# Optimization experiments

Measured on AMD Instinct MI355X. Metric: run time of the kernel, lower is better.

Reference implementation:

```python
import jax, jax.numpy as jnp
import numpy as np

B, T, C = 4, 2048, 2048
N_HEAD = 16
HEAD_DIM = C // N_HEAD
ROPE_BASE = 10000.0


def setup_inputs() -> dict:
    key = jax.random.key(0)
    k1, k2, k3 = jax.random.split(key, 3)
    x = jax.random.normal(k1, (B, T, C), dtype=jnp.float32)
    w_attn = jax.random.normal(k2, (3 * C, C), dtype=jnp.float32) * (1.0 / np.sqrt(C))
    w_proj = jax.random.normal(k3, (C, C), dtype=jnp.float32) * (1.0 / np.sqrt(C))
    return {"x": x, "w_attn": w_attn, "w_proj": w_proj}


def _apply_rope(x, cos, sin):
    # x: [B, H, T, hd]; interleaved pairs (even, odd) rotated
    x_ = x.reshape(*x.shape[:-1], -1, 2)
    x0, x1 = x_[..., 0], x_[..., 1]
    x0r = x0 * cos - x1 * sin
    x1r = x0 * sin + x1 * cos
    return jnp.stack([x0r, x1r], axis=-1).reshape(x.shape)


def reference(x, w_attn, w_proj):
    Bx, Tx, Cx = x.shape
    hd = Cx // N_HEAD
    d = hd // 2

    qkv = jnp.einsum('btc,fc->btf', x, w_attn)  # [B,T,3C]
    q, k, v = jnp.split(qkv, 3, axis=-1)

    def to_heads(t):
        return t.reshape(Bx, Tx, N_HEAD, hd).transpose(0, 2, 1, 3)  # [B,H,T,hd]

    q, k, v = to_heads(q), to_heads(k), to_heads(v)

    # RoPE
    theta = 1.0 / (ROPE_BASE ** (2.0 * jnp.arange(d, dtype=jnp.float32) / hd))
    t = jnp.arange(Tx, dtype=x.dtype)
    freqs = jnp.outer(t, theta.astype(x.dtype))  # [T, d]
    cos = jnp.cos(freqs)[None, None]  # [1,1,T,d]
    sin = jnp.sin(freqs)[None, None]
    q = _apply_rope(q, cos, sin)
    k = _apply_rope(k, cos, sin)

    # Causal attention
    scale = 1.0 / jnp.sqrt(jnp.asarray(hd, dtype=x.dtype))
    scores = jnp.einsum('bhqd,bhkd->bhqk', q, k) * scale
    causal = jnp.tril(jnp.ones((Tx, Tx), dtype=bool))
    scores = jnp.where(causal[None, None], scores, jnp.asarray(-jnp.inf, dtype=scores.dtype))
    attn = jax.nn.softmax(scores, axis=-1)
    y = jnp.einsum('bhqk,bhkd->bhqd', attn, v)  # [B,H,T,hd]

    y = y.transpose(0, 2, 1, 3).reshape(Bx, Tx, Cx)
    return jnp.einsum('btc,oc->bto', y, w_proj)
```

## Files before the change

kernel.cpp:

```cpp
#include <hip/hip_runtime.h>

#define B_ 4
#define T_ 2048
#define C_ 2048
#define H_ 16
#define N1_ 6144
#define M_ 8192
#define SCALE_ 0.08838834764831845f

typedef unsigned short u16;
typedef __bf16 bf16x8 __attribute__((ext_vector_type(8)));
typedef float f32x4 __attribute__((ext_vector_type(4)));
typedef float f32x16 __attribute__((ext_vector_type(16)));

__device__ __forceinline__ u16 f2bf(float f) {
  union { float f; unsigned u; } v; v.f = f;
  return (u16)((v.u + 0x7fffu + ((v.u >> 16) & 1u)) >> 16);
}
__device__ __forceinline__ float bf2f(u16 h) {
  union { unsigned u; float f; } v; v.u = ((unsigned)h) << 16;
  return v.f;
}

__device__ __forceinline__ void gld16(const void* g, void* l) {
  __builtin_amdgcn_global_load_lds(
      (__attribute__((address_space(1))) unsigned int*)(unsigned long long)g,
      (__attribute__((address_space(3))) unsigned int*)(unsigned)(unsigned long long)l,
      16, 0, 0);
}

__global__ void k_cast(const float* __restrict__ in, u16* __restrict__ out, int n4) {
  int i = blockIdx.x * 256 + threadIdx.x;
  if (i >= n4) return;
  float4 v = reinterpret_cast<const float4*>(in)[i];
  ushort4 o;
  o.x = f2bf(v.x); o.y = f2bf(v.y); o.z = f2bf(v.z); o.w = f2bf(v.w);
  reinterpret_cast<ushort4*>(out)[i] = o;
}

__global__ void k_trig(float2* __restrict__ trig) {
  int idx = blockIdx.x * 256 + threadIdx.x;
  int t = idx >> 6, i = idx & 63;
  float theta = __expf(-(float)i * 0.14391156831212787f);
  float f = (float)t * theta;
  float s, c;
  sincosf(f, &s, &c);
  trig[idx] = make_float2(c, s);
}

__global__ void k_rope(u16* __restrict__ qh, u16* __restrict__ kh,
                       const float2* __restrict__ trig) {
  int idx = blockIdx.x * 256 + threadIdx.x;
  u16* base = (idx >> 21) ? kh : qh;
  int c = idx & ((1 << 21) - 1);
  int t = (c >> 4) & (T_ - 1);
  int i0 = (c & 15) << 2;
  u16* p = base + ((size_t)c << 3);
  ushort4 a = *reinterpret_cast<ushort4*>(p);
  ushort4 bq = *reinterpret_cast<ushort4*>(p + 4);
  const float2* tr = trig + t * 64 + i0;
  float2 t0 = tr[0], t1 = tr[1], t2 = tr[2], t3 = tr[3];
  float x0, x1;
  ushort4 ra, rb;
  x0 = bf2f(a.x); x1 = bf2f(a.y);
  ra.x = f2bf(x0 * t0.x - x1 * t0.y); ra.y = f2bf(x0 * t0.y + x1 * t0.x);
  x0 = bf2f(a.z); x1 = bf2f(a.w);
  ra.z = f2bf(x0 * t1.x - x1 * t1.y); ra.w = f2bf(x0 * t1.y + x1 * t1.x);
  x0 = bf2f(bq.x); x1 = bf2f(bq.y);
  rb.x = f2bf(x0 * t2.x - x1 * t2.y); rb.y = f2bf(x0 * t2.y + x1 * t2.x);
  x0 = bf2f(bq.z); x1 = bf2f(bq.w);
  rb.z = f2bf(x0 * t3.x - x1 * t3.y); rb.w = f2bf(x0 * t3.y + x1 * t3.x);
  *reinterpret_cast<ushort4*>(p) = ra;
  *reinterpret_cast<ushort4*>(p + 4) = rb;
}

template <int EPI>
__global__ __launch_bounds__(256, 2) void k_gemm(
    const u16* __restrict__ A, const u16* __restrict__ Bt,
    float* __restrict__ Cf,
    u16* __restrict__ qh, u16* __restrict__ kh, u16* __restrict__ vt,
    int Ndim, int K) {
  __shared__ alignas(16) u16 lA[128 * 32];
  __shared__ alignas(16) u16 lB[128 * 32];
  const int tid = threadIdx.x;
  const int lane = tid & 63;
  const int w = tid >> 6;
  const int wr = w >> 1, wc = w & 1;
  const int l15 = lane & 15, lq = lane >> 4;
  const long rowBase = (long)blockIdx.y * 128;
  const long colBase = (long)blockIdx.x * 128;

  const f32x4 z4 = {0.f, 0.f, 0.f, 0.f};
  f32x4 acc[4][4];
#pragma unroll
  for (int m = 0; m < 4; ++m)
#pragma unroll
    for (int n = 0; n < 4; ++n) acc[m][n] = z4;

  for (int k0 = 0; k0 < K; k0 += 32) {
#pragma unroll
    for (int i = 0; i < 2; ++i) {
      int c = tid + i * 256;
      int r = c >> 2, e = (c & 3) << 3;
      gld16(A + (rowBase + r) * (long)K + k0 + e, (char*)lA + c * 16);
      gld16(Bt + (colBase + r) * (long)K + k0 + e, (char*)lB + c * 16);
    }
    __syncthreads();
    bf16x8 aF[4], bF[4];
#pragma unroll
    for (int m = 0; m < 4; ++m)
      aF[m] = *reinterpret_cast<const bf16x8*>(&lA[(wr * 64 + m * 16 + l15) * 32 + lq * 8]);
#pragma unroll
    for (int n = 0; n < 4; ++n)
      bF[n] = *reinterpret_cast<const bf16x8*>(&lB[(wc * 64 + n * 16 + l15) * 32 + lq * 8]);
#pragma unroll
    for (int m = 0; m < 4; ++m)
#pragma unroll
      for (int n = 0; n < 4; ++n)
        acc[m][n] = __builtin_amdgcn_mfma_f32_16x16x32_bf16(aF[m], bF[n], acc[m][n], 0, 0, 0);
    __syncthreads();
  }

  if (EPI == 0) {
#pragma unroll
    for (int m = 0; m < 4; ++m) {
      long row0 = rowBase + wr * 64 + m * 16 + lq * 4;
#pragma unroll
      for (int n = 0; n < 4; ++n) {
        long col = colBase + wc * 64 + n * 16 + l15;
#pragma unroll
        for (int j = 0; j < 4; ++j)
          Cf[(row0 + j) * (long)Ndim + col] = acc[m][n][j];
      }
    }
  } else {
    const int sec = (int)(colBase >> 11);
    const int hh = ((int)colBase >> 7) & 15;
#pragma unroll
    for (int m = 0; m < 4; ++m) {
      int row0 = (int)rowBase + wr * 64 + m * 16 + lq * 4;
      int b = row0 >> 11;
      int t0 = row0 & (T_ - 1);
      long bh = (long)b * H_ + hh;
#pragma unroll
      for (int n = 0; n < 4; ++n) {
        int dd = wc * 64 + n * 16 + l15;
        if (sec < 2) {
          u16* dst = sec ? kh : qh;
#pragma unroll
          for (int j = 0; j < 4; ++j)
            dst[(bh * T_ + t0 + j) * 128 + dd] = f2bf(acc[m][n][j]);
        } else {
          ushort4 pk;
          pk.x = f2bf(acc[m][n][0]); pk.y = f2bf(acc[m][n][1]);
          pk.z = f2bf(acc[m][n][2]); pk.w = f2bf(acc[m][n][3]);
          *reinterpret_cast<ushort4*>(&vt[(bh * 128 + dd) * T_ + t0]) = pk;
        }
      }
    }
  }
}

#define PACK_SLOT(dst, P, base)                                                       \
  {                                                                                   \
    unsigned ua, ub, uc, ud;                                                          \
    asm("v_cvt_pk_bf16_f32 %0, %1, %2" : "=v"(ua) : "v"(P[base + 0]), "v"(P[base + 1])); \
    asm("v_cvt_pk_bf16_f32 %0, %1, %2" : "=v"(ub) : "v"(P[base + 4]), "v"(P[base + 5])); \
    asm("v_permlane32_swap_b32 %0, %1" : "+v"(ua), "+v"(ub));                         \
    asm("v_cvt_pk_bf16_f32 %0, %1, %2" : "=v"(uc) : "v"(P[base + 2]), "v"(P[base + 3])); \
    asm("v_cvt_pk_bf16_f32 %0, %1, %2" : "=v"(ud) : "v"(P[base + 6]), "v"(P[base + 7])); \
    asm("v_permlane32_swap_b32 %0, %1" : "+v"(uc), "+v"(ud));                         \
    union { unsigned u[4]; bf16x8 v; } tt;                                            \
    tt.u[0] = ua; tt.u[1] = uc; tt.u[2] = ub; tt.u[3] = ud;                           \
    dst = tt.v;                                                                       \
  }

__global__ __launch_bounds__(256, 2) void k_attn(
    const u16* __restrict__ qh, const u16* __restrict__ kh,
    const u16* __restrict__ vt, u16* __restrict__ ym) {
  __shared__ alignas(16) u16 lK[2][64 * 128];
  __shared__ alignas(16) u16 lV[2][128 * 64];
  const int tid = threadIdx.x;
  const int lane = tid & 63;
  const int w = tid >> 6;
  const int l31 = lane & 31;
  const int hi = lane >> 5;
  const int swz = (l31 & 7) << 4;
  const int id = (int)blockIdx.x;
  const int pr = id >> 6;
  const int bh = ((id & 7) << 3) | ((id >> 3) & 7);
  const int b = bh >> 4, hh = bh & 15;
  const u16* Kbase = kh + (long)bh * T_ * 128;
  const u16* Vbase = vt + (long)bh * 128 * T_;
  const u16* Qbase = qh + (long)bh * T_ * 128;

  auto stage = [&](int bi, int t0) {
#pragma unroll
    for (int i = 0; i < 4; ++i) {
      int c = tid + i * 256;
      int rK = c >> 4;
      int lbK = ((c & 15) << 4) ^ ((rK & 7) << 4);
      gld16(Kbase + (long)(t0 + rK) * 128 + (lbK >> 1), (char*)(&lK[bi][0]) + c * 16);
      int dV = c >> 3;
      int lbV = ((c & 7) << 4) ^ ((dV & 7) << 4);
      gld16(Vbase + (long)dV * T_ + t0 + (lbV >> 1), (char*)(&lV[bi][0]) + c * 16);
    }
  };

#pragma unroll 1
  for (int half = 0; half < 2; ++half) {
    const int p = half ? 15 - pr : pr;
    const int NT = 2 * (p + 1);
    const int qw = p * 128 + w * 32;
    const int ntw = (qw + 95) >> 6;

    bf16x8 qF[8];
    {
      const u16* qrow = Qbase + (long)(qw + l31) * 128 + hi * 8;
#pragma unroll
      for (int s = 0; s < 8; ++s)
        qF[s] = *reinterpret_cast<const bf16x8*>(qrow + s * 16);
    }

    f32x16 oA[4];
#pragma unroll
    for (int n = 0; n < 4; ++n)
#pragma unroll
      for (int r = 0; r < 16; ++r) oA[n][r] = 0.f;
    float mR = -1e30f, lR = 0.f;

    stage(0, 0);
    __syncthreads();
    int cur = 0;
#pragma unroll 1
    for (int jt = 0; jt < NT; ++jt) {
      if (jt + 1 < NT) stage(cur ^ 1, (jt + 1) * 64);
      if (jt < ntw) {
        const int t0 = jt * 64;
        const char* Kc = (const char*)(&lK[cur][0]);
        const char* Vc = (const char*)(&lV[cur][0]);
        f32x16 s0, s1;
#pragma unroll
        for (int r = 0; r < 16; ++r) { s0[r] = 0.f; s1[r] = 0.f; }
        __builtin_amdgcn_s_setprio(1);
#pragma unroll
        for (int s = 0; s < 8; ++s) {
          int cb = (s * 32 + hi * 16) ^ swz;
          bf16x8 k0 = *reinterpret_cast<const bf16x8*>(Kc + l31 * 256 + cb);
          bf16x8 k1 = *reinterpret_cast<const bf16x8*>(Kc + (32 + l31) * 256 + cb);
          s0 = __builtin_amdgcn_mfma_f32_32x32x16_bf16(k0, qF[s], s0, 0, 0, 0);
          s1 = __builtin_amdgcn_mfma_f32_32x32x16_bf16(k1, qF[s], s1, 0, 0, 0);
        }
        __builtin_amdgcn_s_setprio(0);

        float f0[16], f1[16];
#pragma unroll
        for (int r = 0; r < 16; ++r) { f0[r] = s0[r] * SCALE_; f1[r] = s1[r] * SCALE_; }
        if (jt == ntw - 1) {
          const int qa = qw + l31;
#pragma unroll
          for (int r = 0; r < 16; ++r) {
            int kv = t0 + (r & 3) + 8 * (r >> 2) + 4 * hi;
            if (kv > qa) f0[r] = -1e30f;
            if (kv + 32 > qa) f1[r] = -1e30f;
          }
        }
        float mt = fmaxf(f0[0], f1[0]);
#pragma unroll
        for (int r = 1; r < 16; ++r) mt = fmaxf(mt, fmaxf(f0[r], f1[r]));
        mt = fmaxf(mt, __shfl_xor(mt, 32));
        float mN = fmaxf(mR, mt);
        float al = __expf(mR - mN);
        mR = mN;
        float rs = 0.f;
#pragma unroll
        for (int r = 0; r < 16; ++r) {
          f0[r] = __expf(f0[r] - mN);
          f1[r] = __expf(f1[r] - mN);
          rs += f0[r] + f1[r];
        }
        rs += __shfl_xor(rs, 32);
        lR = lR * al + rs;
        float aR[16];
#pragma unroll
        for (int r = 0; r < 16; ++r)
          aR[r] = __shfl(al, (r & 3) + 8 * (r >> 2) + 4 * hi);
#pragma unroll
        for (int n = 0; n < 4; ++n)
#pragma unroll
          for (int r = 0; r < 16; ++r) oA[n][r] *= aR[r];

        bf16x8 paF[4];
        PACK_SLOT(paF[0], f0, 0);
        PACK_SLOT(paF[1], f0, 8);
        PACK_SLOT(paF[2], f1, 0);
        PACK_SLOT(paF[3], f1, 8);

        __builtin_amdgcn_s_setprio(1);
#pragma unroll
        for (int n = 0; n < 4; ++n) {
          const char* vrow = Vc + (n * 32 + l31) * 128;
#pragma unroll
          for (int ks = 0; ks < 4; ++ks) {
            bf16x8 bV = *reinterpret_cast<const bf16x8*>(vrow + ((ks * 32 + hi * 16) ^ swz));
            oA[n] = __builtin_amdgcn_mfma_f32_32x32x16_bf16(paF[ks], bV, oA[n], 0, 0, 0);
          }
        }
        __builtin_amdgcn_s_setprio(0);
      }
      __syncthreads();
      cur ^= 1;
    }

    float li = 1.f / lR;
    float liR[16];
#pragma unroll
    for (int r = 0; r < 16; ++r)
      liR[r] = __shfl(li, (r & 3) + 8 * (r >> 2) + 4 * hi);
    u16* yrow = ym + ((long)b * T_ + qw) * C_ + hh * 128 + l31;
#pragma unroll
    for (int n = 0; n < 4; ++n)
#pragma unroll
      for (int r = 0; r < 16; ++r) {
        int cr = (r & 3) + 8 * (r >> 2) + 4 * hi;
        yrow[(long)cr * C_ + n * 32] = f2bf(oA[n][r] * liR[r]);
      }
  }
}

extern "C" void kernel_launch(void* const* d_in, const int* in_sizes, int n_in,
                              void* d_out, int out_size, void* d_ws, size_t ws_size,
                              hipStream_t stream) {
  (void)in_sizes; (void)n_in; (void)out_size; (void)ws_size;
  const float* x = (const float*)d_in[0];
  const float* wa = (const float*)d_in[1];
  const float* wp = (const float*)d_in[2];
  float* out = (float*)d_out;
  char* ws = (char*)d_ws;

  size_t off = 0;
  auto alloc = [&](size_t bytes) -> char* {
    char* p = ws + off;
    off += (bytes + 255) & ~(size_t)255;
    return p;
  };
  u16* xb  = (u16*)alloc((size_t)M_ * C_ * 2);
  u16* wab = (u16*)alloc((size_t)N1_ * C_ * 2);
  u16* wpb = (u16*)alloc((size_t)C_ * C_ * 2);
  u16* qh  = (u16*)alloc((size_t)64 * T_ * 128 * 2);
  u16* kh  = (u16*)alloc((size_t)64 * T_ * 128 * 2);
  u16* vt  = (u16*)alloc((size_t)64 * 128 * T_ * 2);
  float2* trig = (float2*)alloc((size_t)T_ * 64 * 8);
  u16* ym = xb;

  k_cast<<<dim3((M_ * C_ / 4) / 256), 256, 0, stream>>>(x, xb, M_ * C_ / 4);
  k_cast<<<dim3((N1_ * C_ / 4) / 256), 256, 0, stream>>>(wa, wab, N1_ * C_ / 4);
  k_cast<<<dim3((C_ * C_ / 4) / 256), 256, 0, stream>>>(wp, wpb, C_ * C_ / 4);
  k_trig<<<dim3((T_ * 64) / 256), 256, 0, stream>>>(trig);
  k_gemm<1><<<dim3(N1_ / 128, M_ / 128), 256, 0, stream>>>(
      xb, wab, nullptr, qh, kh, vt, N1_, C_);
  k_rope<<<dim3((2 * 64 * T_ * 16) / 256), 256, 0, stream>>>(qh, kh, trig);
  k_attn<<<dim3(512), 256, 0, stream>>>(qh, kh, vt, ym);
  k_gemm<0><<<dim3(C_ / 128, M_ / 128), 256, 0, stream>>>(
      ym, wpb, out, nullptr, nullptr, nullptr, C_, C_);
}
```

Baseline: 493.6 us.

## Rewrite GEMM as 256x128 triple-buffered pipelined kernel and fuse RoPE into epilogue

Replaces the 128x128, single-buffered, 32-wide-K GEMM with an 8-wave 256x128 tile. It uses a 3-stage LDS ring over 64-wide K slices, issues async global-to-LDS loads interleaved with MFMA phases, and controls ordering with explicit vmcnt waits, barriers and s_setprio. LDS rows are XOR-swizzled to avoid bank conflicts, and blocks are remapped with a grouped swizzle to improve L2 reuse. RoPE is folded into the QKV GEMM epilogue using a lane-pair shuffle, which removes the separate read-modify-write rope kernel. The kernel now hardcodes K=2048 and uses about 144KB of LDS per block, which limits occupancy to one block per CU.

```diff
diff --git a/kernel.cpp b/kernel.cpp
--- a/kernel.cpp
+++ b/kernel.cpp
@@ -48,47 +48,28 @@
   trig[idx] = make_float2(c, s);
 }
 
-__global__ void k_rope(u16* __restrict__ qh, u16* __restrict__ kh,
-                       const float2* __restrict__ trig) {
-  int idx = blockIdx.x * 256 + threadIdx.x;
-  u16* base = (idx >> 21) ? kh : qh;
-  int c = idx & ((1 << 21) - 1);
-  int t = (c >> 4) & (T_ - 1);
-  int i0 = (c & 15) << 2;
-  u16* p = base + ((size_t)c << 3);
-  ushort4 a = *reinterpret_cast<ushort4*>(p);
-  ushort4 bq = *reinterpret_cast<ushort4*>(p + 4);
-  const float2* tr = trig + t * 64 + i0;
-  float2 t0 = tr[0], t1 = tr[1], t2 = tr[2], t3 = tr[3];
-  float x0, x1;
-  ushort4 ra, rb;
-  x0 = bf2f(a.x); x1 = bf2f(a.y);
-  ra.x = f2bf(x0 * t0.x - x1 * t0.y); ra.y = f2bf(x0 * t0.y + x1 * t0.x);
-  x0 = bf2f(a.z); x1 = bf2f(a.w);
-  ra.z = f2bf(x0 * t1.x - x1 * t1.y); ra.w = f2bf(x0 * t1.y + x1 * t1.x);
-  x0 = bf2f(bq.x); x1 = bf2f(bq.y);
-  rb.x = f2bf(x0 * t2.x - x1 * t2.y); rb.y = f2bf(x0 * t2.y + x1 * t2.x);
-  x0 = bf2f(bq.z); x1 = bf2f(bq.w);
-  rb.z = f2bf(x0 * t3.x - x1 * t3.y); rb.w = f2bf(x0 * t3.y + x1 * t3.x);
-  *reinterpret_cast<ushort4*>(p) = ra;
-  *reinterpret_cast<ushort4*>(p + 4) = rb;
-}
-
 template <int EPI>
-__global__ __launch_bounds__(256, 2) void k_gemm(
+__global__ __launch_bounds__(512, 2) void k_gemm8(
     const u16* __restrict__ A, const u16* __restrict__ Bt,
     float* __restrict__ Cf,
     u16* __restrict__ qh, u16* __restrict__ kh, u16* __restrict__ vt,
-    int Ndim, int K) {
-  __shared__ alignas(16) u16 lA[128 * 32];
-  __shared__ alignas(16) u16 lB[128 * 32];
+    const float2* __restrict__ trig, int nbx, int cpx) {
+  __shared__ alignas(16) u16 lA[3 * 256 * 64];
+  __shared__ alignas(16) u16 lB[3 * 128 * 64];
   const int tid = threadIdx.x;
   const int lane = tid & 63;
   const int w = tid >> 6;
   const int wr = w >> 1, wc = w & 1;
   const int l15 = lane & 15, lq = lane >> 4;
-  const long rowBase = (long)blockIdx.y * 128;
-  const long colBase = (long)blockIdx.x * 128;
+  const int rs = l15 & 7;
+
+  const int id = (int)blockIdx.x;
+  const int swz = (id & 7) * cpx + (id >> 3);
+  const int bx = swz % nbx, by = swz / nbx;
+  const long rowBase = (long)by * 256;
+  const long colBase = (long)bx * 128;
+  const u16* Ag = A + rowBase * 2048;
+  const u16* Bg = Bt + colBase * 2048;
 
   const f32x4 z4 = {0.f, 0.f, 0.f, 0.f};
   f32x4 acc[4][4];
@@ -97,28 +78,99 @@
 #pragma unroll
     for (int n = 0; n < 4; ++n) acc[m][n] = z4;
 
-  for (int k0 = 0; k0 < K; k0 += 32) {
-#pragma unroll
-    for (int i = 0; i < 2; ++i) {
-      int c = tid + i * 256;
-      int r = c >> 2, e = (c & 3) << 3;
-      gld16(A + (rowBase + r) * (long)K + k0 + e, (char*)lA + c * 16);
-      gld16(Bt + (colBase + r) * (long)K + k0 + e, (char*)lB + c * 16);
-    }
-    __syncthreads();
+#pragma unroll
+  for (int pt = 0; pt < 2; ++pt) {
+    char* Ad = (char*)lA + pt * 32768;
+    char* Bd = (char*)lB + pt * 16384;
+    const long kG = (long)pt * 64;
+#pragma unroll
+    for (int q = 0; q < 4; ++q) {
+      int c = tid + q * 512;
+      gld16(Ag + (long)(c >> 3) * 2048 + kG + (((c & 7) ^ ((c >> 3) & 7)) << 3),
+            Ad + c * 16);
+    }
+#pragma unroll
+    for (int q = 0; q < 2; ++q) {
+      int c = tid + q * 512;
+      gld16(Bg + (long)(c >> 3) * 2048 + kG + (((c & 7) ^ ((c >> 3) & 7)) << 3),
+            Bd + c * 16);
+    }
+  }
+  asm volatile("s_waitcnt vmcnt(6)" ::: "memory");
+  __builtin_amdgcn_s_barrier();
+
+  int slot = 0;
+#pragma unroll 1
+  for (int t = 0; t < 32; ++t) {
+    const char* As = (const char*)lA + slot * 32768;
+    const char* Bs = (const char*)lB + slot * 16384;
+    int s2 = slot + 2; if (s2 >= 3) s2 -= 3;
+    char* Ad = (char*)lA + s2 * 32768;
+    char* Bd = (char*)lB + s2 * 16384;
+    const long kG = (long)(t + 2) * 64;
+    const bool st = (t < 30);
+
     bf16x8 aF[4], bF[4];
 #pragma unroll
-    for (int m = 0; m < 4; ++m)
-      aF[m] = *reinterpret_cast<const bf16x8*>(&lA[(wr * 64 + m * 16 + l15) * 32 + lq * 8]);
-#pragma unroll
-    for (int n = 0; n < 4; ++n)
-      bF[n] = *reinterpret_cast<const bf16x8*>(&lB[(wc * 64 + n * 16 + l15) * 32 + lq * 8]);
-#pragma unroll
-    for (int m = 0; m < 4; ++m)
-#pragma unroll
-      for (int n = 0; n < 4; ++n)
-        acc[m][n] = __builtin_amdgcn_mfma_f32_16x16x32_bf16(aF[m], bF[n], acc[m][n], 0, 0, 0);
-    __syncthreads();
+    for (int fm = 0; fm < 4; ++fm)
+      aF[fm] = *reinterpret_cast<const bf16x8*>(
+          As + (wr * 64 + fm * 16 + l15) * 128 + ((lq ^ rs) << 4));
+#pragma unroll
+    for (int fn = 0; fn < 4; ++fn)
+      bF[fn] = *reinterpret_cast<const bf16x8*>(
+          Bs + (wc * 64 + fn * 16 + l15) * 128 + ((lq ^ rs) << 4));
+    if (st) {
+#pragma unroll
+      for (int q = 0; q < 3; ++q) {
+        int c = tid + q * 512;
+        gld16(Ag + (long)(c >> 3) * 2048 + kG + (((c & 7) ^ ((c >> 3) & 7)) << 3),
+              Ad + c * 16);
+      }
+    }
+    __builtin_amdgcn_s_barrier();
+    __builtin_amdgcn_s_setprio(1);
+#pragma unroll
+    for (int fm = 0; fm < 4; ++fm)
+#pragma unroll
+      for (int fn = 0; fn < 4; ++fn)
+        acc[fm][fn] =
+            __builtin_amdgcn_mfma_f32_16x16x32_bf16(aF[fm], bF[fn], acc[fm][fn], 0, 0, 0);
+    __builtin_amdgcn_s_setprio(0);
+    __builtin_amdgcn_s_barrier();
+#pragma unroll
+    for (int fm = 0; fm < 4; ++fm)
+      aF[fm] = *reinterpret_cast<const bf16x8*>(
+          As + (wr * 64 + fm * 16 + l15) * 128 + (((4 | lq) ^ rs) << 4));
+#pragma unroll
+    for (int fn = 0; fn < 4; ++fn)
+      bF[fn] = *reinterpret_cast<const bf16x8*>(
+          Bs + (wc * 64 + fn * 16 + l15) * 128 + (((4 | lq) ^ rs) << 4));
+    if (st) {
+      {
+        int c = tid + 1536;
+        gld16(Ag + (long)(c >> 3) * 2048 + kG + (((c & 7) ^ ((c >> 3) & 7)) << 3),
+              Ad + c * 16);
+      }
+#pragma unroll
+      for (int q = 0; q < 2; ++q) {
+        int c = tid + q * 512;
+        gld16(Bg + (long)(c >> 3) * 2048 + kG + (((c & 7) ^ ((c >> 3) & 7)) << 3),
+              Bd + c * 16);
+      }
+    }
+    __builtin_amdgcn_s_barrier();
+    __builtin_amdgcn_s_setprio(1);
+#pragma unroll
+    for (int fm = 0; fm < 4; ++fm)
+#pragma unroll
+      for (int fn = 0; fn < 4; ++fn)
+        acc[fm][fn] =
+            __builtin_amdgcn_mfma_f32_16x16x32_bf16(aF[fm], bF[fn], acc[fm][fn], 0, 0, 0);
+    __builtin_amdgcn_s_setprio(0);
+    if (st) asm volatile("s_waitcnt vmcnt(6)" ::: "memory");
+    else    asm volatile("s_waitcnt vmcnt(0)" ::: "memory");
+    __builtin_amdgcn_s_barrier();
+    slot = (slot == 2) ? 0 : slot + 1;
   }
 
   if (EPI == 0) {
@@ -130,7 +182,7 @@
         long col = colBase + wc * 64 + n * 16 + l15;
 #pragma unroll
         for (int j = 0; j < 4; ++j)
-          Cf[(row0 + j) * (long)Ndim + col] = acc[m][n][j];
+          Cf[(row0 + j) * 2048 + col] = acc[m][n][j];
       }
     }
   } else {
@@ -148,8 +200,13 @@
         if (sec < 2) {
           u16* dst = sec ? kh : qh;
 #pragma unroll
-          for (int j = 0; j < 4; ++j)
-            dst[(bh * T_ + t0 + j) * 128 + dd] = f2bf(acc[m][n][j]);
+          for (int j = 0; j < 4; ++j) {
+            float v = acc[m][n][j];
+            float vp = __shfl_xor(v, 1);
+            float2 cs = trig[(t0 + j) * 64 + (dd >> 1)];
+            float r = (dd & 1) ? (vp * cs.y + v * cs.x) : (v * cs.x - vp * cs.y);
+            dst[(bh * T_ + t0 + j) * 128 + dd] = f2bf(r);
+          }
         } else {
           ushort4 pk;
           pk.x = f2bf(acc[m][n][0]); pk.y = f2bf(acc[m][n][1]);
@@ -357,10 +414,9 @@
   k_cast<<<dim3((N1_ * C_ / 4) / 256), 256, 0, stream>>>(wa, wab, N1_ * C_ / 4);
   k_cast<<<dim3((C_ * C_ / 4) / 256), 256, 0, stream>>>(wp, wpb, C_ * C_ / 4);
   k_trig<<<dim3((T_ * 64) / 256), 256, 0, stream>>>(trig);
-  k_gemm<1><<<dim3(N1_ / 128, M_ / 128), 256, 0, stream>>>(
-      xb, wab, nullptr, qh, kh, vt, N1_, C_);
-  k_rope<<<dim3((2 * 64 * T_ * 16) / 256), 256, 0, stream>>>(qh, kh, trig);
+  k_gemm8<1><<<dim3(1536), 512, 0, stream>>>(
+      xb, wab, nullptr, qh, kh, vt, trig, 48, 192);
   k_attn<<<dim3(512), 256, 0, stream>>>(qh, kh, vt, ym);
-  k_gemm<0><<<dim3(C_ / 128, M_ / 128), 256, 0, stream>>>(
-      ym, wpb, out, nullptr, nullptr, nullptr, C_, C_);
-}
+  k_gemm8<0><<<dim3(512), 512, 0, stream>>>(
+      ym, wpb, out, nullptr, nullptr, nullptr, nullptr, 16, 64);
+}
```

After: 463.3 us. -6.1%, faster.

## Replace GEMMs with 256x256 double-buffered pipelined kernel and fuse RoPE epilogue

Applied to the files above, without the earlier changes.

Replaces the simple 128x128 single-stage GEMM with a 512-thread 256x256 tile kernel using 64-wide K tiles, XOR-swizzled LDS, double-buffered async global-to-LDS staging interleaved with MFMA phases, s_setprio, and a grouped block-index swizzle for L2 reuse. RoPE is folded into the QKV GEMM epilogue using lane shuffles to fetch the pair partner, removing the separate rope kernel and its extra read/write pass over q and k. This trades much higher register and LDS pressure (128 KB LDS per block) and hardcoded K=2048 for better data reuse and latency hiding.

```diff
diff --git a/kernel.cpp b/kernel.cpp
--- a/kernel.cpp
+++ b/kernel.cpp
@@ -48,112 +48,144 @@
   trig[idx] = make_float2(c, s);
 }
 
-__global__ void k_rope(u16* __restrict__ qh, u16* __restrict__ kh,
-                       const float2* __restrict__ trig) {
-  int idx = blockIdx.x * 256 + threadIdx.x;
-  u16* base = (idx >> 21) ? kh : qh;
-  int c = idx & ((1 << 21) - 1);
-  int t = (c >> 4) & (T_ - 1);
-  int i0 = (c & 15) << 2;
-  u16* p = base + ((size_t)c << 3);
-  ushort4 a = *reinterpret_cast<ushort4*>(p);
-  ushort4 bq = *reinterpret_cast<ushort4*>(p + 4);
-  const float2* tr = trig + t * 64 + i0;
-  float2 t0 = tr[0], t1 = tr[1], t2 = tr[2], t3 = tr[3];
-  float x0, x1;
-  ushort4 ra, rb;
-  x0 = bf2f(a.x); x1 = bf2f(a.y);
-  ra.x = f2bf(x0 * t0.x - x1 * t0.y); ra.y = f2bf(x0 * t0.y + x1 * t0.x);
-  x0 = bf2f(a.z); x1 = bf2f(a.w);
-  ra.z = f2bf(x0 * t1.x - x1 * t1.y); ra.w = f2bf(x0 * t1.y + x1 * t1.x);
-  x0 = bf2f(bq.x); x1 = bf2f(bq.y);
-  rb.x = f2bf(x0 * t2.x - x1 * t2.y); rb.y = f2bf(x0 * t2.y + x1 * t2.x);
-  x0 = bf2f(bq.z); x1 = bf2f(bq.w);
-  rb.z = f2bf(x0 * t3.x - x1 * t3.y); rb.w = f2bf(x0 * t3.y + x1 * t3.x);
-  *reinterpret_cast<ushort4*>(p) = ra;
-  *reinterpret_cast<ushort4*>(p + 4) = rb;
-}
+
+#define STAGE_H(BUF, AB, HALF, KT, GSH)                                          \
+  {                                                                              \
+    _Pragma("unroll") for (int q = 0; q < 2; ++q) {                              \
+      int c = tid + q * 512;                                                     \
+      int idx = c >> 3;                                                          \
+      int row = (idx & ((1 << (GSH)) - 1)) + ((HALF) << (GSH)) +                 \
+                ((idx >> (GSH)) << ((GSH) + 1));                                 \
+      gld16(((AB) ? Bg : Ag) + (long)row * 2048 + (long)(KT) * 64 +              \
+                (((c & 7) ^ (idx & 7)) << 3),                                    \
+            (char*)&lds[BUF][AB][row * 64 + (c & 7) * 8]);                       \
+    }                                                                            \
+  }
+
+#define PHASE(BUF, MH, NH, RDA, RDB, STAGE_CODE, WAIT_CODE)                      \
+  {                                                                              \
+    if (RDA) {                                                                   \
+      _Pragma("unroll") for (int fr = 0; fr < 4; ++fr)                           \
+        _Pragma("unroll") for (int ks = 0; ks < 2; ++ks)                         \
+          aCur[fr][ks] = *reinterpret_cast<const bf16x8*>(                       \
+              &lds[BUF][0][(wm * 128 + (MH) * 64 + fr * 16 + l15) * 64 +         \
+                           (((ks * 4 + lq) ^ swl) << 3)]);                       \
+    }                                                                            \
+    if (RDB) {                                                                   \
+      _Pragma("unroll") for (int fc = 0; fc < 2; ++fc)                           \
+        _Pragma("unroll") for (int ks = 0; ks < 2; ++ks)                         \
+          bKp[NH][fc][ks] = *reinterpret_cast<const bf16x8*>(                    \
+              &lds[BUF][1][(wn * 64 + (NH) * 32 + fc * 16 + l15) * 64 +          \
+                           (((ks * 4 + lq) ^ swl) << 3)]);                       \
+    }                                                                            \
+    STAGE_CODE;                                                                  \
+    __builtin_amdgcn_s_barrier();                                                \
+    __builtin_amdgcn_s_setprio(1);                                               \
+    _Pragma("unroll") for (int fr = 0; fr < 4; ++fr)                             \
+      _Pragma("unroll") for (int fc = 0; fc < 2; ++fc)                           \
+        _Pragma("unroll") for (int ks = 0; ks < 2; ++ks)                         \
+          acc[(MH) * 4 + fr][(NH) * 2 + fc] =                                    \
+              __builtin_amdgcn_mfma_f32_16x16x32_bf16(                           \
+                  aCur[fr][ks], bKp[NH][fc][ks],                                 \
+                  acc[(MH) * 4 + fr][(NH) * 2 + fc], 0, 0, 0);                   \
+    __builtin_amdgcn_s_setprio(0);                                               \
+    WAIT_CODE;                                                                   \
+    __builtin_amdgcn_s_barrier();                                                \
+  }
 
 template <int EPI>
-__global__ __launch_bounds__(256, 2) void k_gemm(
+__global__ __launch_bounds__(512, 2) void k_gemm8(
     const u16* __restrict__ A, const u16* __restrict__ Bt,
     float* __restrict__ Cf,
     u16* __restrict__ qh, u16* __restrict__ kh, u16* __restrict__ vt,
-    int Ndim, int K) {
-  __shared__ alignas(16) u16 lA[128 * 32];
-  __shared__ alignas(16) u16 lB[128 * 32];
+    const float2* __restrict__ trig, int nbx, int cpx) {
+  __shared__ alignas(16) u16 lds[2][2][256 * 64];
   const int tid = threadIdx.x;
   const int lane = tid & 63;
   const int w = tid >> 6;
-  const int wr = w >> 1, wc = w & 1;
+  const int wm = w >> 2;
+  const int wn = w & 3;
   const int l15 = lane & 15, lq = lane >> 4;
-  const long rowBase = (long)blockIdx.y * 128;
-  const long colBase = (long)blockIdx.x * 128;
+  const int swl = l15 & 7;
+
+  const int id = (int)blockIdx.x;
+  const int swz = (id & 7) * cpx + (id >> 3);
+  const int bx = swz % nbx, by = swz / nbx;
+  const long rowBase = (long)by * 256;
+  const long colBase = (long)bx * 256;
+  const u16* Ag = A + rowBase * 2048;
+  const u16* Bg = Bt + colBase * 2048;
 
   const f32x4 z4 = {0.f, 0.f, 0.f, 0.f};
-  f32x4 acc[4][4];
-#pragma unroll
-  for (int m = 0; m < 4; ++m)
+  f32x4 acc[8][4];
+#pragma unroll
+  for (int m = 0; m < 8; ++m)
 #pragma unroll
     for (int n = 0; n < 4; ++n) acc[m][n] = z4;
-
-  for (int k0 = 0; k0 < K; k0 += 32) {
-#pragma unroll
-    for (int i = 0; i < 2; ++i) {
-      int c = tid + i * 256;
-      int r = c >> 2, e = (c & 3) << 3;
-      gld16(A + (rowBase + r) * (long)K + k0 + e, (char*)lA + c * 16);
-      gld16(Bt + (colBase + r) * (long)K + k0 + e, (char*)lB + c * 16);
-    }
-    __syncthreads();
-    bf16x8 aF[4], bF[4];
-#pragma unroll
-    for (int m = 0; m < 4; ++m)
-      aF[m] = *reinterpret_cast<const bf16x8*>(&lA[(wr * 64 + m * 16 + l15) * 32 + lq * 8]);
-#pragma unroll
-    for (int n = 0; n < 4; ++n)
-      bF[n] = *reinterpret_cast<const bf16x8*>(&lB[(wc * 64 + n * 16 + l15) * 32 + lq * 8]);
-#pragma unroll
-    for (int m = 0; m < 4; ++m)
-#pragma unroll
-      for (int n = 0; n < 4; ++n)
-        acc[m][n] = __builtin_amdgcn_mfma_f32_16x16x32_bf16(aF[m], bF[n], acc[m][n], 0, 0, 0);
-    __syncthreads();
+  bf16x8 aCur[4][2], bKp[2][2][2];
+
+  STAGE_H(0, 0, 0, 0, 6); STAGE_H(0, 1, 0, 0, 5);
+  STAGE_H(0, 0, 1, 0, 6); STAGE_H(0, 1, 1, 0, 5);
+  STAGE_H(1, 0, 0, 1, 6); STAGE_H(1, 1, 0, 1, 5);
+  asm volatile("s_waitcnt vmcnt(4)" ::: "memory");
+  __builtin_amdgcn_s_barrier();
+
+#pragma unroll 1
+  for (int i = 0; i < 16; ++i) {
+    const int t1 = 2 * i + 1, t2 = 2 * i + 2, t3 = 2 * i + 3;
+    const bool st = (i < 15);
+    PHASE(0, 0, 0, 1, 1, STAGE_H(1, 0, 1, t1, 6), );
+    PHASE(0, 0, 1, 0, 1, STAGE_H(1, 1, 1, t1, 5), );
+    PHASE(0, 1, 0, 1, 0, if (st) STAGE_H(0, 0, 0, t2, 6), );
+    PHASE(0, 1, 1, 0, 0, if (st) STAGE_H(0, 1, 0, t2, 5),
+          if (st) { asm volatile("s_waitcnt vmcnt(4)" ::: "memory"); }
+          else    { asm volatile("s_waitcnt vmcnt(0)" ::: "memory"); });
+    PHASE(1, 0, 0, 1, 1, if (st) STAGE_H(0, 0, 1, t2, 6), );
+    PHASE(1, 0, 1, 0, 1, if (st) STAGE_H(0, 1, 1, t2, 5), );
+    PHASE(1, 1, 0, 1, 0, if (st) STAGE_H(1, 0, 0, t3, 6), );
+    PHASE(1, 1, 1, 0, 0, if (st) STAGE_H(1, 1, 0, t3, 5),
+          if (st) { asm volatile("s_waitcnt vmcnt(4)" ::: "memory"); });
   }
 
   if (EPI == 0) {
 #pragma unroll
-    for (int m = 0; m < 4; ++m) {
-      long row0 = rowBase + wr * 64 + m * 16 + lq * 4;
-#pragma unroll
-      for (int n = 0; n < 4; ++n) {
-        long col = colBase + wc * 64 + n * 16 + l15;
+    for (int fr = 0; fr < 8; ++fr) {
+      long row0 = rowBase + wm * 128 + fr * 16 + lq * 4;
+#pragma unroll
+      for (int fc = 0; fc < 4; ++fc) {
+        long col = colBase + wn * 64 + fc * 16 + l15;
 #pragma unroll
         for (int j = 0; j < 4; ++j)
-          Cf[(row0 + j) * (long)Ndim + col] = acc[m][n][j];
+          Cf[(row0 + j) * 2048 + col] = acc[fr][fc][j];
       }
     }
   } else {
     const int sec = (int)(colBase >> 11);
-    const int hh = ((int)colBase >> 7) & 15;
-#pragma unroll
-    for (int m = 0; m < 4; ++m) {
-      int row0 = (int)rowBase + wr * 64 + m * 16 + lq * 4;
+#pragma unroll
+    for (int fr = 0; fr < 8; ++fr) {
+      int row0 = (int)rowBase + wm * 128 + fr * 16 + lq * 4;
       int b = row0 >> 11;
       int t0 = row0 & (T_ - 1);
-      long bh = (long)b * H_ + hh;
-#pragma unroll
-      for (int n = 0; n < 4; ++n) {
-        int dd = wc * 64 + n * 16 + l15;
+#pragma unroll
+      for (int fc = 0; fc < 4; ++fc) {
+        int cc = (int)colBase + wn * 64 + fc * 16;
+        int hh = (cc >> 7) & 15;
+        int dd = (cc & 127) + l15;
+        long bh = (long)b * H_ + hh;
         if (sec < 2) {
           u16* dst = sec ? kh : qh;
 #pragma unroll
-          for (int j = 0; j < 4; ++j)
-            dst[(bh * T_ + t0 + j) * 128 + dd] = f2bf(acc[m][n][j]);
+          for (int j = 0; j < 4; ++j) {
+            float v = acc[fr][fc][j];
+            float vp = __shfl_xor(v, 1);
+            float2 cs = trig[(t0 + j) * 64 + (dd >> 1)];
+            float r = (dd & 1) ? (vp * cs.y + v * cs.x) : (v * cs.x - vp * cs.y);
+            dst[(bh * T_ + t0 + j) * 128 + dd] = f2bf(r);
+          }
         } else {
           ushort4 pk;
-          pk.x = f2bf(acc[m][n][0]); pk.y = f2bf(acc[m][n][1]);
-          pk.z = f2bf(acc[m][n][2]); pk.w = f2bf(acc[m][n][3]);
+          pk.x = f2bf(acc[fr][fc][0]); pk.y = f2bf(acc[fr][fc][1]);
+          pk.z = f2bf(acc[fr][fc][2]); pk.w = f2bf(acc[fr][fc][3]);
           *reinterpret_cast<ushort4*>(&vt[(bh * 128 + dd) * T_ + t0]) = pk;
         }
       }
@@ -357,10 +389,9 @@
   k_cast<<<dim3((N1_ * C_ / 4) / 256), 256, 0, stream>>>(wa, wab, N1_ * C_ / 4);
   k_cast<<<dim3((C_ * C_ / 4) / 256), 256, 0, stream>>>(wp, wpb, C_ * C_ / 4);
   k_trig<<<dim3((T_ * 64) / 256), 256, 0, stream>>>(trig);
-  k_gemm<1><<<dim3(N1_ / 128, M_ / 128), 256, 0, stream>>>(
-      xb, wab, nullptr, qh, kh, vt, N1_, C_);
-  k_rope<<<dim3((2 * 64 * T_ * 16) / 256), 256, 0, stream>>>(qh, kh, trig);
+  k_gemm8<1><<<dim3(768), 512, 0, stream>>>(
+      xb, wab, nullptr, qh, kh, vt, trig, 24, 96);
   k_attn<<<dim3(512), 256, 0, stream>>>(qh, kh, vt, ym);
-  k_gemm<0><<<dim3(C_ / 128, M_ / 128), 256, 0, stream>>>(
-      ym, wpb, out, nullptr, nullptr, nullptr, C_, C_);
-}
+  k_gemm8<0><<<dim3(256), 512, 0, stream>>>(
+      ym, wpb, out, nullptr, nullptr, nullptr, nullptr, 8, 32);
+}
```

After: 414.2 us. -16.1%, faster.
